# Optimization experiments

Measured on AMD Instinct MI355X. Metric: run time of the kernel, lower is better.

The kernel has to match this reference:

```python
import jax, jax.numpy as jnp
import numpy as np

N, E, F, H, L, G = 100000, 1600000, 32, 128, 4, 64


def gru_cell(m, h, w_ih, b_ih, w_hh, b_hh):
    # torch.nn.GRUCell math; gate order: r, z, n
    gi = m @ w_ih.T + b_ih          # [N, 3H]
    gh = h @ w_hh.T + b_hh          # [N, 3H]
    i_r, i_z, i_n = jnp.split(gi, 3, axis=-1)
    h_r, h_z, h_n = jnp.split(gh, 3, axis=-1)
    r = jax.nn.sigmoid(i_r + h_r)
    z = jax.nn.sigmoid(i_z + h_z)
    n = jnp.tanh(i_n + r * h_n)
    return (1.0 - z) * n + z * h


def setup_inputs() -> dict:
    key = jax.random.key(0)
    ks = jax.random.split(key, 12)
    s = 0.05
    return {
        "x": jax.random.normal(ks[0], (N, F), jnp.float32),
        "edge_index": jax.random.randint(ks[1], (2, E), 0, N, jnp.int64),
        "batch": jnp.sort(jax.random.randint(ks[2], (N,), 0, G, jnp.int64)),
        "num_graphs": G,
        "W0": jax.random.normal(ks[3], (H, F), jnp.float32) * s,
        "conv_w": jax.random.normal(ks[4], (L, H, H), jnp.float32) * s,
        "w_ih": jax.random.normal(ks[5], (3 * H, H), jnp.float32) * s,
        "b_ih": jax.random.normal(ks[6], (3 * H,), jnp.float32) * s,
        "w_hh": jax.random.normal(ks[7], (3 * H, H), jnp.float32) * s,
        "b_hh": jax.random.normal(ks[8], (3 * H,), jnp.float32) * s,
        "lin1_w": jax.random.normal(ks[9], (1, H), jnp.float32) * s,
        "lin1_b": jax.random.normal(ks[10], (1,), jnp.float32) * s,
    }


def reference(x, edge_index, batch, num_graphs, W0, conv_w, w_ih, b_ih, w_hh, b_hh, lin1_w, lin1_b):
    n_nodes = x.shape[0]
    # lin0 (no bias) + sigmoid embedding
    x_embed = jax.nn.sigmoid(x @ W0.T)                     # [N, H]

    src, dst = edge_index[0], edge_index[1]
    h = x_embed
    # GatedGraphConv: per layer, transform -> scatter-add over edges -> GRU update
    for l in range(conv_w.shape[0]):
        m = h @ conv_w[l]                                   # [N, H]
        agg = jax.ops.segment_sum(m[src], dst, num_segments=n_nodes)  # [N, H]
        h = gru_cell(agg, h, w_ih, b_ih, w_hh, b_hh)

    h = jax.nn.relu(h)
    out = h @ lin1_w.T + lin1_b                             # [N, 1]
    uncorrected = out

    # per-graph mean subtraction (scatter_mean + gather), same math as the loop
    sums = jax.ops.segment_sum(out, batch, num_segments=num_graphs)   # [G, 1]
    counts = jax.ops.segment_sum(jnp.ones((n_nodes, 1), out.dtype), batch, num_segments=num_graphs)
    mean_all = sums / jnp.maximum(counts, 1.0)
    corrected = out - mean_all[batch]

    return corrected.squeeze(1), x_embed, uncorrected.squeeze(1)
```

## Files before the change

### kernel.cpp

```cpp
#include <hip/hip_runtime.h>
#include <hip/hip_bf16.h>

#define HDIM 128
#define FDIM 32
#define GGR  64
#define SCAN_CHUNK 2048
#define FILL_CHUNK 1024
#define FILL_WIN 16

typedef __attribute__((ext_vector_type(8))) short bf16x8;
typedef __attribute__((ext_vector_type(4))) float f32x4;

__device__ __forceinline__ float fsig(float x) {
  return __builtin_amdgcn_rcpf(1.f + __expf(-x));
}
__device__ __forceinline__ float ftanh(float x) {
  return 1.f - 2.f * __builtin_amdgcn_rcpf(1.f + __expf(2.f * x));
}

__device__ __forceinline__ bf16x8 pack_bf16x8(float4 a, float4 b) {
  union { bf16x8 v; __hip_bfloat162 h[4]; } u;
  u.h[0] = __float22bfloat162_rn(make_float2(a.x, a.y));
  u.h[1] = __float22bfloat162_rn(make_float2(a.z, a.w));
  u.h[2] = __float22bfloat162_rn(make_float2(b.x, b.y));
  u.h[3] = __float22bfloat162_rn(make_float2(b.z, b.w));
  return u.v;
}

__device__ __forceinline__ int ablk(int kb, int m) {
  return (kb << 6) + (m & 56) + ((m ^ kb) & 7);
}

__device__ __forceinline__ void stage64(const unsigned short* __restrict__ g,
                                        short* __restrict__ s, int n0, int N, int t) {
#pragma unroll
  for (int r = 0; r < 2; ++r) {
    int idx = r * 512 + t;
    int m = idx >> 4, c8 = idx & 15;
    int gn = n0 + m;
    uint4 v = make_uint4(0u, 0u, 0u, 0u);
    if (gn < N) v = *(const uint4*)(g + (size_t)gn * HDIM + c8 * 8);
    *(uint4*)(s + ablk(c8, m) * 8) = v;
  }
}

__global__ __launch_bounds__(256) void k_embed_mfma(const float* __restrict__ x,
                                                    const unsigned short* __restrict__ W0b,
                                                    unsigned short* __restrict__ hb,
                                                    float* __restrict__ xemb,
                                                    const unsigned short* __restrict__ convT0,
                                                    unsigned short* __restrict__ m_out,
                                                    int N) {
  __shared__ short sE[16 * 64 * 8];
  int t = threadIdx.x;
  int w = t >> 6, l = t & 63;
  int lm = l & 15, lq = l >> 4;
  int n0 = blockIdx.x * 64;
  int j0 = w * 32;
  bf16x8 b0 = *(const bf16x8*)(W0b + (size_t)(j0 + lm) * FDIM + lq * 8);
  bf16x8 b1 = *(const bf16x8*)(W0b + (size_t)(j0 + 16 + lm) * FDIM + lq * 8);
  f32x4 acc0[4], acc1[4];
#pragma unroll
  for (int i = 0; i < 4; ++i) { acc0[i] = (f32x4){0.f,0.f,0.f,0.f}; acc1[i] = (f32x4){0.f,0.f,0.f,0.f}; }
#pragma unroll
  for (int tt = 0; tt < 4; ++tt) {
    int rg = n0 + tt * 16 + lm;
    bf16x8 a = (bf16x8){0,0,0,0,0,0,0,0};
    if (rg < N) {
      const float4* xr = (const float4*)x + (size_t)rg * 8 + lq * 2;
      a = pack_bf16x8(xr[0], xr[1]);
    }
    acc0[tt] = __builtin_amdgcn_mfma_f32_16x16x32_bf16(a, b0, acc0[tt], 0, 0, 0);
    acc1[tt] = __builtin_amdgcn_mfma_f32_16x16x32_bf16(a, b1, acc1[tt], 0, 0, 0);
  }
#pragma unroll
  for (int g = 0; g < 2; ++g) {
    int j = j0 + g * 16 + lm;
#pragma unroll
    for (int tt = 0; tt < 4; ++tt)
#pragma unroll
      for (int r = 0; r < 4; ++r) {
        int m = tt * 16 + lq * 4 + r;
        int node = n0 + m;
        float v = g ? acc1[tt][r] : acc0[tt][r];
        float e = fsig(v);
        __hip_bfloat16 eb = __float2bfloat16(e);
        ((__hip_bfloat16*)sE)[ablk(j >> 3, m) * 8 + (j & 7)] = eb;
        if (node < N) {
          size_t off = (size_t)node * HDIM + j;
          xemb[off] = e;
          ((__hip_bfloat16*)hb)[off] = eb;
        }
      }
  }
  __syncthreads();
#pragma unroll
  for (int g = 0; g < 2; ++g) {
    int jg = j0 + g * 16;
    f32x4 macc[4];
#pragma unroll
    for (int i = 0; i < 4; ++i) macc[i] = (f32x4){0.f,0.f,0.f,0.f};
#pragma unroll
    for (int ks = 0; ks < 4; ++ks) {
      bf16x8 b = *(const bf16x8*)(convT0 + (size_t)(jg + lm) * HDIM + ks * 32 + lq * 8);
      int kb = ks * 4 + lq;
#pragma unroll
      for (int tt = 0; tt < 4; ++tt) {
        bf16x8 a = *(const bf16x8*)(sE + ablk(kb, tt * 16 + lm) * 8);
        macc[tt] = __builtin_amdgcn_mfma_f32_16x16x32_bf16(a, b, macc[tt], 0, 0, 0);
      }
    }
    int j = jg + lm;
#pragma unroll
    for (int tt = 0; tt < 4; ++tt)
#pragma unroll
      for (int r = 0; r < 4; ++r) {
        int node = n0 + tt * 16 + lq * 4 + r;
        if (node < N)
          ((__hip_bfloat16*)m_out)[(size_t)node * HDIM + j] = __float2bfloat16(macc[tt][r]);
      }
  }
}

__global__ __launch_bounds__(256) void k_prep_w(const float* __restrict__ w_ih,
                                                const float* __restrict__ w_hh,
                                                const float* __restrict__ conv_w,
                                                const float* __restrict__ W0,
                                                unsigned short* __restrict__ wIb,
                                                unsigned short* __restrict__ wHb,
                                                unsigned short* __restrict__ convTb,
                                                unsigned short* __restrict__ W0b,
                                                int L) {
  int i = blockIdx.x * 256 + threadIdx.x;
  if (i < HDIM * FDIM) ((__hip_bfloat16*)W0b)[i] = __float2bfloat16(W0[i]);
  if (i < 384 * HDIM) {
    ((__hip_bfloat16*)wIb)[i] = __float2bfloat16(w_ih[i]);
    ((__hip_bfloat16*)wHb)[i] = __float2bfloat16(w_hh[i]);
  }
  int total = L * HDIM * HDIM;
  if (i < total) {
    int l = i >> 14, rem = i & 16383, j = rem >> 7, k = rem & 127;
    ((__hip_bfloat16*)convTb)[i] = __float2bfloat16(conv_w[(l << 14) + (k << 7) + j]);
  }
}

__global__ __launch_bounds__(256) void k_hist(const int* __restrict__ dst, int* __restrict__ deg,
                                              unsigned short* __restrict__ rank,
                                              long long E) {
  long long e = (long long)blockIdx.x * 256 + threadIdx.x;
  if (e < E) {
    int old = atomicAdd(&deg[dst[e]], 1);
    rank[e] = (unsigned short)old;
  }
}

__global__ __launch_bounds__(256) void k_block_sum(const int* __restrict__ deg,
                                                   int* __restrict__ bsum, int N) {
  int base = blockIdx.x * SCAN_CHUNK + threadIdx.x * 8;
  int s = 0;
#pragma unroll
  for (int u = 0; u < 8; ++u) { int i = base + u; if (i < N) s += deg[i]; }
#pragma unroll
  for (int o = 32; o; o >>= 1) s += __shfl_down(s, o, 64);
  __shared__ int wsum[4];
  if ((threadIdx.x & 63) == 0) wsum[threadIdx.x >> 6] = s;
  __syncthreads();
  if (threadIdx.x == 0) bsum[blockIdx.x] = wsum[0] + wsum[1] + wsum[2] + wsum[3];
}

__global__ void k_scan_bsums(int* __restrict__ bsum, int nb) {
  if (blockIdx.x == 0 && threadIdx.x == 0) {
    int run = 0;
    for (int i = 0; i < nb; ++i) { int v = bsum[i]; bsum[i] = run; run += v; }
  }
}

__global__ __launch_bounds__(256) void k_scan_chunks(const int* __restrict__ deg,
                                                     const int* __restrict__ bsum,
                                                     int* __restrict__ rowstart,
                                                     int N, int Etot) {
  __shared__ int ts[256];
  int base = blockIdx.x * SCAN_CHUNK + threadIdx.x * 8;
  int loc[8]; int s = 0;
#pragma unroll
  for (int u = 0; u < 8; ++u) {
    int i = base + u; loc[u] = s;
    s += (i < N) ? deg[i] : 0;
  }
  ts[threadIdx.x] = s;
  __syncthreads();
  for (int o = 1; o < 256; o <<= 1) {
    int v = (threadIdx.x >= o) ? ts[threadIdx.x - o] : 0;
    __syncthreads();
    ts[threadIdx.x] += v;
    __syncthreads();
  }
  int texcl = (threadIdx.x ? ts[threadIdx.x - 1] : 0) + bsum[blockIdx.x];
#pragma unroll
  for (int u = 0; u < 8; ++u) {
    int i = base + u;
    if (i < N) rowstart[i] = texcl + loc[u];
  }
  if (blockIdx.x == 0 && threadIdx.x == 0) rowstart[N] = Etot;
}

__global__ __launch_bounds__(256) void k_csr_fill_win(const int* __restrict__ src,
                                                      const int* __restrict__ dst,
                                                      const unsigned short* __restrict__ rank,
                                                      const int* __restrict__ rowstart,
                                                      int* __restrict__ csr,
                                                      long long E, int N) {
  __shared__ int sd[FILL_CHUNK];
  __shared__ int ss[FILL_CHUNK];
  __shared__ unsigned short sr[FILL_CHUNK];
  long long base = (long long)blockIdx.x * FILL_CHUNK;
  int cnt = (int)((E - base < FILL_CHUNK) ? (E - base) : FILL_CHUNK);
  for (int i = threadIdx.x; i < cnt; i += 256) {
    sd[i] = dst[base + i];
    ss[i] = src[base + i];
    sr[i] = rank[base + i];
  }
  __syncthreads();
  int nw = (N + FILL_WIN - 1) / FILL_WIN;
#pragma unroll 1
  for (int w = 0; w < FILL_WIN; ++w) {
    int lo = w * nw, hi = lo + nw;
    for (int i = threadIdx.x; i < cnt; i += 256) {
      int d = sd[i];
      if (d >= lo && d < hi)
        csr[rowstart[d] + sr[i]] = ss[i];
    }
    __syncthreads();
  }
}

__global__ __launch_bounds__(256) void k_gather(const int* __restrict__ csr,
                                                const int* __restrict__ rowstart,
                                                const unsigned short* __restrict__ m,
                                                unsigned short* __restrict__ agg, int N) {
  int wv = threadIdx.x >> 6, l = threadIdx.x & 63;
  int n = blockIdx.x * 4 + wv;
  if (n >= N) return;
  int eq = l >> 4;
  int jb = l & 15;
  int beg = rowstart[n], end = rowstart[n + 1];
  float acc[8] = {0.f, 0.f, 0.f, 0.f, 0.f, 0.f, 0.f, 0.f};
  for (int e0 = beg; e0 < end; e0 += 4) {
    int e = e0 + eq;
    uint4 v = make_uint4(0u, 0u, 0u, 0u);
    if (e < end) {
      int s = csr[e];
      v = *(const uint4*)(m + (size_t)s * HDIM + jb * 8);
    }
    acc[0] += __uint_as_float(v.x << 16);
    acc[1] += __uint_as_float(v.x & 0xffff0000u);
    acc[2] += __uint_as_float(v.y << 16);
    acc[3] += __uint_as_float(v.y & 0xffff0000u);
    acc[4] += __uint_as_float(v.z << 16);
    acc[5] += __uint_as_float(v.z & 0xffff0000u);
    acc[6] += __uint_as_float(v.w << 16);
    acc[7] += __uint_as_float(v.w & 0xffff0000u);
  }
#pragma unroll
  for (int i = 0; i < 8; ++i) {
    acc[i] += __shfl_xor(acc[i], 16, 64);
    acc[i] += __shfl_xor(acc[i], 32, 64);
  }
  if (eq == 0) {
    union { uint4 v; __hip_bfloat162 h[4]; } o;
#pragma unroll
    for (int i = 0; i < 4; ++i)
      o.h[i] = __float22bfloat162_rn(make_float2(acc[2 * i], acc[2 * i + 1]));
    *(uint4*)(agg + (size_t)n * HDIM + jb * 8) = o.v;
  }
}

__global__ __launch_bounds__(512) void k_gru_mfma(const unsigned short* __restrict__ aggb,
                                                  const unsigned short* __restrict__ hb,
                                                  const unsigned short* __restrict__ wI,
                                                  const unsigned short* __restrict__ wH,
                                                  const float* __restrict__ b_ih,
                                                  const float* __restrict__ b_hh,
                                                  unsigned short* __restrict__ hnewb,
                                                  const unsigned short* __restrict__ wT,
                                                  unsigned short* __restrict__ m_out,
                                                  int N) {
  __shared__ short sAg[16 * 64 * 8];
  __shared__ short sH[16 * 64 * 8];
  int t = threadIdx.x;
  int n0 = blockIdx.x * 64;
  stage64(aggb, sAg, n0, N, t);
  stage64(hb, sH, n0, N, t);
  int w = t >> 6, l = t & 63;
  int j0 = w * 16;
  int lm = l & 15, lq = l >> 4;
  int j = j0 + lm;
  float bir = b_ih[j], biz = b_ih[j + 128], bin = b_ih[j + 256];
  float bhr = b_hh[j], bhz = b_hh[j + 128], bhn = b_hh[j + 256];
  __syncthreads();
  f32x4 aIR[4], aIZ[4], aIN[4], aHR[4], aHZ[4], aHN[4];
#pragma unroll
  for (int i = 0; i < 4; ++i) {
    aIR[i] = (f32x4){0.f,0.f,0.f,0.f}; aIZ[i] = (f32x4){0.f,0.f,0.f,0.f};
    aIN[i] = (f32x4){0.f,0.f,0.f,0.f}; aHR[i] = (f32x4){0.f,0.f,0.f,0.f};
    aHZ[i] = (f32x4){0.f,0.f,0.f,0.f}; aHN[i] = (f32x4){0.f,0.f,0.f,0.f};
  }
#pragma unroll
  for (int ks = 0; ks < 4; ++ks) {
    size_t rI = (size_t)(j0 + lm) * HDIM + ks * 32 + lq * 8;
    bf16x8 bIr = *(const bf16x8*)(wI + rI);
    bf16x8 bIz = *(const bf16x8*)(wI + rI + 128 * HDIM);
    bf16x8 bIn = *(const bf16x8*)(wI + rI + 256 * HDIM);
    bf16x8 bHr = *(const bf16x8*)(wH + rI);
    bf16x8 bHz = *(const bf16x8*)(wH + rI + 128 * HDIM);
    bf16x8 bHn = *(const bf16x8*)(wH + rI + 256 * HDIM);
    int kb = ks * 4 + lq;
#pragma unroll
    for (int tt = 0; tt < 4; ++tt) {
      bf16x8 a = *(const bf16x8*)(sAg + ablk(kb, tt * 16 + lm) * 8);
      bf16x8 h = *(const bf16x8*)(sH + ablk(kb, tt * 16 + lm) * 8);
      aIR[tt] = __builtin_amdgcn_mfma_f32_16x16x32_bf16(a, bIr, aIR[tt], 0, 0, 0);
      aIZ[tt] = __builtin_amdgcn_mfma_f32_16x16x32_bf16(a, bIz, aIZ[tt], 0, 0, 0);
      aIN[tt] = __builtin_amdgcn_mfma_f32_16x16x32_bf16(a, bIn, aIN[tt], 0, 0, 0);
      aHR[tt] = __builtin_amdgcn_mfma_f32_16x16x32_bf16(h, bHr, aHR[tt], 0, 0, 0);
      aHZ[tt] = __builtin_amdgcn_mfma_f32_16x16x32_bf16(h, bHz, aHZ[tt], 0, 0, 0);
      aHN[tt] = __builtin_amdgcn_mfma_f32_16x16x32_bf16(h, bHn, aHN[tt], 0, 0, 0);
    }
  }
  __syncthreads();
#pragma unroll
  for (int tt = 0; tt < 4; ++tt)
#pragma unroll
    for (int r = 0; r < 4; ++r) {
      int m = tt * 16 + lq * 4 + r;
      int node = n0 + m;
      float hp = __bfloat162float(((const __hip_bfloat16*)sH)[ablk(j >> 3, m) * 8 + (j & 7)]);
      float rg = fsig(aIR[tt][r] + bir + aHR[tt][r] + bhr);
      float zg = fsig(aIZ[tt][r] + biz + aHZ[tt][r] + bhz);
      float nv = aIN[tt][r] + bin + rg * (aHN[tt][r] + bhn);
      float th = ftanh(nv);
      float hn = (1.f - zg) * th + zg * hp;
      __hip_bfloat16 hnb = __float2bfloat16(hn);
      ((__hip_bfloat16*)sAg)[ablk(j >> 3, m) * 8 + (j & 7)] = hnb;
      if (node < N)
        ((__hip_bfloat16*)hnewb)[(size_t)node * HDIM + j] = hnb;
    }
  if (wT) {
    __syncthreads();
    f32x4 macc[4];
#pragma unroll
    for (int i = 0; i < 4; ++i) macc[i] = (f32x4){0.f,0.f,0.f,0.f};
#pragma unroll
    for (int ks = 0; ks < 4; ++ks) {
      bf16x8 b = *(const bf16x8*)(wT + (size_t)(j0 + lm) * HDIM + ks * 32 + lq * 8);
      int kb = ks * 4 + lq;
#pragma unroll
      for (int tt = 0; tt < 4; ++tt) {
        bf16x8 a = *(const bf16x8*)(sAg + ablk(kb, tt * 16 + lm) * 8);
        macc[tt] = __builtin_amdgcn_mfma_f32_16x16x32_bf16(a, b, macc[tt], 0, 0, 0);
      }
    }
#pragma unroll
    for (int tt = 0; tt < 4; ++tt)
#pragma unroll
      for (int r = 0; r < 4; ++r) {
        int node = n0 + tt * 16 + lq * 4 + r;
        if (node < N)
          ((__hip_bfloat16*)m_out)[(size_t)node * HDIM + j] = __float2bfloat16(macc[tt][r]);
      }
  }
}

__global__ __launch_bounds__(256) void k_readout(const unsigned short* __restrict__ h,
                                                 const float* __restrict__ w1,
                                                 const float* __restrict__ b1,
                                                 float* __restrict__ out_raw,
                                                 float* __restrict__ uncorrected,
                                                 int N) {
  int wave = threadIdx.x >> 6;
  int lane = threadIdx.x & 63;
  int n = blockIdx.x * 4 + wave;
  if (n >= N) return;
  float h0 = __bfloat162float(((const __hip_bfloat16*)h)[(size_t)n * HDIM + lane]);
  float h1 = __bfloat162float(((const __hip_bfloat16*)h)[(size_t)n * HDIM + 64 + lane]);
  float v = fmaxf(h0, 0.f) * w1[lane] + fmaxf(h1, 0.f) * w1[64 + lane];
#pragma unroll
  for (int o = 32; o > 0; o >>= 1) v += __shfl_down(v, o, 64);
  if (lane == 0) {
    float o = v + b1[0];
    out_raw[n] = o;
    uncorrected[n] = o;
  }
}

__global__ __launch_bounds__(256) void k_graph_reduce(const float* __restrict__ out_raw,
                                                      const int* __restrict__ batch,
                                                      float* __restrict__ gsum,
                                                      float* __restrict__ gcnt,
                                                      int N) {
  __shared__ float ls[GGR], lc[GGR];
  int t = threadIdx.x;
  if (t < GGR) { ls[t] = 0.f; lc[t] = 0.f; }
  __syncthreads();
  for (int n = blockIdx.x * 256 + t; n < N; n += gridDim.x * 256) {
    int g = batch[n];
    atomicAdd(&ls[g], out_raw[n]);
    atomicAdd(&lc[g], 1.f);
  }
  __syncthreads();
  if (t < GGR) {
    unsafeAtomicAdd(&gsum[t], ls[t]);
    unsafeAtomicAdd(&gcnt[t], lc[t]);
  }
}

__global__ __launch_bounds__(256) void k_correct(const float* __restrict__ out_raw,
                                                 const int* __restrict__ batch,
                                                 const float* __restrict__ gsum,
                                                 const float* __restrict__ gcnt,
                                                 float* __restrict__ corrected, int N) {
  int n = blockIdx.x * 256 + threadIdx.x;
  if (n < N) {
    int g = batch[n];
    corrected[n] = out_raw[n] - gsum[g] / fmaxf(gcnt[g], 1.f);
  }
}

extern "C" void kernel_launch(void* const* d_in, const int* in_sizes, int n_in,
                              void* d_out, int out_size, void* d_ws, size_t ws_size,
                              hipStream_t stream) {
  const float* x      = (const float*)d_in[0];
  const int*   ei     = (const int*)d_in[1];
  const int*   batch  = (const int*)d_in[2];
  const float* W0     = (const float*)d_in[4];
  const float* conv_w = (const float*)d_in[5];
  const float* w_ih   = (const float*)d_in[6];
  const float* b_ih   = (const float*)d_in[7];
  const float* w_hh   = (const float*)d_in[8];
  const float* b_hh   = (const float*)d_in[9];
  const float* lin1_w = (const float*)d_in[10];
  const float* lin1_b = (const float*)d_in[11];

  int N = in_sizes[0] / FDIM;
  long long E = in_sizes[1] / 2;
  int L = in_sizes[5] / (HDIM * HDIM);

  const int* src = ei;
  const int* dstv = ei + E;

  float* out_corrected = (float*)d_out;
  float* out_xemb = out_corrected + N;
  float* out_unc  = out_xemb + (size_t)N * HDIM;

  char* p = (char*)d_ws;
  unsigned short* x0 = (unsigned short*)p; p += (size_t)N * HDIM * 2;
  unsigned short* x1 = (unsigned short*)p; p += (size_t)N * HDIM * 2;
  unsigned short* x2 = (unsigned short*)p; p += (size_t)N * HDIM * 2;
  float* out_raw = (float*)p;        p += (size_t)((N + 3) & ~3) * 4;
  float* gsum = (float*)p;           p += GGR * 4;
  float* gcnt = (float*)p;           p += GGR * 4;
  int* deg = (int*)p;                p += (size_t)((N + 3) & ~3) * 4;
  int* rowstart = (int*)p;           p += (size_t)(N + 4) * 4;
  int nb = (N + SCAN_CHUNK - 1) / SCAN_CHUNK;
  int* bsum = (int*)p;               p += (size_t)((nb + 63) & ~63) * 4;
  int* csr = (int*)p;                p += (size_t)E * 4;
  unsigned short* rankb = (unsigned short*)p;  p += (size_t)((E + 3) & ~3) * 2;
  unsigned short* wIb = (unsigned short*)p;    p += 384 * HDIM * 2;
  unsigned short* wHb = (unsigned short*)p;    p += 384 * HDIM * 2;
  unsigned short* convTb = (unsigned short*)p; p += (size_t)L * HDIM * HDIM * 2;
  unsigned short* W0b = (unsigned short*)p;

  int prep_total = (384 * HDIM > L * HDIM * HDIM) ? 384 * HDIM : L * HDIM * HDIM;
  k_prep_w<<<(prep_total + 255) / 256, 256, 0, stream>>>(w_ih, w_hh, conv_w, W0, wIb, wHb, convTb, W0b, L);

  hipMemsetAsync(deg, 0, (size_t)N * sizeof(int), stream);
  k_hist<<<(int)((E + 255) / 256), 256, 0, stream>>>(dstv, deg, rankb, E);
  k_block_sum<<<nb, 256, 0, stream>>>(deg, bsum, N);
  k_scan_bsums<<<1, 64, 0, stream>>>(bsum, nb);
  k_scan_chunks<<<nb, 256, 0, stream>>>(deg, bsum, rowstart, N, (int)E);
  k_csr_fill_win<<<(int)((E + FILL_CHUNK - 1) / FILL_CHUNK), 256, 0, stream>>>(
      src, dstv, rankb, rowstart, csr, E, N);

  int nblk = (N + 63) / 64;
  k_embed_mfma<<<nblk, 256, 0, stream>>>(x, W0b, x0, out_xemb, convTb, x1, N);

  unsigned short* Hb = x0;
  unsigned short* Mb = x1;
  for (int l = 0; l < L; ++l) {
    k_gather<<<(N + 3) / 4, 256, 0, stream>>>(csr, rowstart, Mb, x2, N);
    const unsigned short* wTn = (l + 1 < L) ? (convTb + (size_t)(l + 1) * HDIM * HDIM) : nullptr;
    k_gru_mfma<<<nblk, 512, 0, stream>>>(x2, Hb, wIb, wHb, b_ih, b_hh, Mb, wTn, Hb, N);
    unsigned short* tmp = Hb; Hb = Mb; Mb = tmp;
  }

  hipMemsetAsync(gsum, 0, 2 * GGR * sizeof(float), stream);
  k_readout<<<(N + 3) / 4, 256, 0, stream>>>(Hb, lin1_w, lin1_b, out_raw, out_unc, N);
  k_graph_reduce<<<256, 256, 0, stream>>>(out_raw, batch, gsum, gcnt, N);
  k_correct<<<(N + 255) / 256, 256, 0, stream>>>(out_raw, batch, gsum, gcnt, out_corrected, N);
}
```

Measured before the change: 844.9 us.

## Fuse histogram into embed kernel; merge GRU accumulators and raise occupancy

```diff
diff --git a/kernel.cpp b/kernel.cpp
--- a/kernel.cpp
+++ b/kernel.cpp
@@ -44,18 +44,31 @@
   }
 }
 
-__global__ __launch_bounds__(256) void k_embed_mfma(const float* __restrict__ x,
+__global__ __launch_bounds__(256) void k_embed_hist(const float* __restrict__ x,
                                                     const unsigned short* __restrict__ W0b,
                                                     unsigned short* __restrict__ hb,
                                                     float* __restrict__ xemb,
                                                     const unsigned short* __restrict__ convT0,
                                                     unsigned short* __restrict__ m_out,
-                                                    int N) {
+                                                    int N,
+                                                    const int* __restrict__ dst,
+                                                    int* __restrict__ deg,
+                                                    unsigned short* __restrict__ rank,
+                                                    long long E, int histBlocks) {
   __shared__ short sE[16 * 64 * 8];
+  if ((int)blockIdx.x < histBlocks) {
+    long long e = (long long)blockIdx.x * 256 + threadIdx.x;
+    if (e < E) {
+      int old = atomicAdd(&deg[dst[e]], 1);
+      rank[e] = (unsigned short)old;
+    }
+    return;
+  }
+  int bid = blockIdx.x - histBlocks;
   int t = threadIdx.x;
   int w = t >> 6, l = t & 63;
   int lm = l & 15, lq = l >> 4;
-  int n0 = blockIdx.x * 64;
+  int n0 = bid * 64;
   int j0 = w * 32;
   bf16x8 b0 = *(const bf16x8*)(W0b + (size_t)(j0 + lm) * FDIM + lq * 8);
   bf16x8 b1 = *(const bf16x8*)(W0b + (size_t)(j0 + 16 + lm) * FDIM + lq * 8);
@@ -141,16 +154,6 @@
   if (i < total) {
     int l = i >> 14, rem = i & 16383, j = rem >> 7, k = rem & 127;
     ((__hip_bfloat16*)convTb)[i] = __float2bfloat16(conv_w[(l << 14) + (k << 7) + j]);
-  }
-}
-
-__global__ __launch_bounds__(256) void k_hist(const int* __restrict__ dst, int* __restrict__ deg,
-                                              unsigned short* __restrict__ rank,
-                                              long long E) {
-  long long e = (long long)blockIdx.x * 256 + threadIdx.x;
-  if (e < E) {
-    int old = atomicAdd(&deg[dst[e]], 1);
-    rank[e] = (unsigned short)old;
   }
 }
 
@@ -275,7 +278,7 @@
   }
 }
 
-__global__ __launch_bounds__(512) void k_gru_mfma(const unsigned short* __restrict__ aggb,
+__global__ __launch_bounds__(512, 4) void k_gru_mfma(const unsigned short* __restrict__ aggb,
                                                   const unsigned short* __restrict__ hb,
                                                   const unsigned short* __restrict__ wI,
                                                   const unsigned short* __restrict__ wH,
@@ -298,12 +301,11 @@
   float bir = b_ih[j], biz = b_ih[j + 128], bin = b_ih[j + 256];
   float bhr = b_hh[j], bhz = b_hh[j + 128], bhn = b_hh[j + 256];
   __syncthreads();
-  f32x4 aIR[4], aIZ[4], aIN[4], aHR[4], aHZ[4], aHN[4];
+  f32x4 aR[4], aZ[4], aNi[4], aNh[4];
 #pragma unroll
   for (int i = 0; i < 4; ++i) {
-    aIR[i] = (f32x4){0.f,0.f,0.f,0.f}; aIZ[i] = (f32x4){0.f,0.f,0.f,0.f};
-    aIN[i] = (f32x4){0.f,0.f,0.f,0.f}; aHR[i] = (f32x4){0.f,0.f,0.f,0.f};
-    aHZ[i] = (f32x4){0.f,0.f,0.f,0.f}; aHN[i] = (f32x4){0.f,0.f,0.f,0.f};
+    aR[i] = (f32x4){0.f,0.f,0.f,0.f}; aZ[i] = (f32x4){0.f,0.f,0.f,0.f};
+    aNi[i] = (f32x4){0.f,0.f,0.f,0.f}; aNh[i] = (f32x4){0.f,0.f,0.f,0.f};
   }
 #pragma unroll
   for (int ks = 0; ks < 4; ++ks) {
@@ -319,12 +321,12 @@
     for (int tt = 0; tt < 4; ++tt) {
       bf16x8 a = *(const bf16x8*)(sAg + ablk(kb, tt * 16 + lm) * 8);
       bf16x8 h = *(const bf16x8*)(sH + ablk(kb, tt * 16 + lm) * 8);
-      aIR[tt] = __builtin_amdgcn_mfma_f32_16x16x32_bf16(a, bIr, aIR[tt], 0, 0, 0);
-      aIZ[tt] = __builtin_amdgcn_mfma_f32_16x16x32_bf16(a, bIz, aIZ[tt], 0, 0, 0);
-      aIN[tt] = __builtin_amdgcn_mfma_f32_16x16x32_bf16(a, bIn, aIN[tt], 0, 0, 0);
-      aHR[tt] = __builtin_amdgcn_mfma_f32_16x16x32_bf16(h, bHr, aHR[tt], 0, 0, 0);
-      aHZ[tt] = __builtin_amdgcn_mfma_f32_16x16x32_bf16(h, bHz, aHZ[tt], 0, 0, 0);
-      aHN[tt] = __builtin_amdgcn_mfma_f32_16x16x32_bf16(h, bHn, aHN[tt], 0, 0, 0);
+      aR[tt] = __builtin_amdgcn_mfma_f32_16x16x32_bf16(a, bIr, aR[tt], 0, 0, 0);
+      aR[tt] = __builtin_amdgcn_mfma_f32_16x16x32_bf16(h, bHr, aR[tt], 0, 0, 0);
+      aZ[tt] = __builtin_amdgcn_mfma_f32_16x16x32_bf16(a, bIz, aZ[tt], 0, 0, 0);
+      aZ[tt] = __builtin_amdgcn_mfma_f32_16x16x32_bf16(h, bHz, aZ[tt], 0, 0, 0);
+      aNi[tt] = __builtin_amdgcn_mfma_f32_16x16x32_bf16(a, bIn, aNi[tt], 0, 0, 0);
+      aNh[tt] = __builtin_amdgcn_mfma_f32_16x16x32_bf16(h, bHn, aNh[tt], 0, 0, 0);
     }
   }
   __syncthreads();
@@ -335,9 +337,9 @@
       int m = tt * 16 + lq * 4 + r;
       int node = n0 + m;
       float hp = __bfloat162float(((const __hip_bfloat16*)sH)[ablk(j >> 3, m) * 8 + (j & 7)]);
-      float rg = fsig(aIR[tt][r] + bir + aHR[tt][r] + bhr);
-      float zg = fsig(aIZ[tt][r] + biz + aHZ[tt][r] + bhz);
-      float nv = aIN[tt][r] + bin + rg * (aHN[tt][r] + bhn);
+      float rg = fsig(aR[tt][r] + bir + bhr);
+      float zg = fsig(aZ[tt][r] + biz + bhz);
+      float nv = aNi[tt][r] + bin + rg * (aNh[tt][r] + bhn);
       float th = ftanh(nv);
       float hn = (1.f - zg) * th + zg * hp;
       __hip_bfloat16 hnb = __float2bfloat16(hn);
@@ -474,15 +476,17 @@
   k_prep_w<<<(prep_total + 255) / 256, 256, 0, stream>>>(w_ih, w_hh, conv_w, W0, wIb, wHb, convTb, W0b, L);
 
   hipMemsetAsync(deg, 0, (size_t)N * sizeof(int), stream);
-  k_hist<<<(int)((E + 255) / 256), 256, 0, stream>>>(dstv, deg, rankb, E);
+
+  int nblk = (N + 63) / 64;
+  int histBlocks = (int)((E + 255) / 256);
+  k_embed_hist<<<histBlocks + nblk, 256, 0, stream>>>(x, W0b, x0, out_xemb, convTb, x1, N,
+                                                      dstv, deg, rankb, E, histBlocks);
+
   k_block_sum<<<nb, 256, 0, stream>>>(deg, bsum, N);
   k_scan_bsums<<<1, 64, 0, stream>>>(bsum, nb);
   k_scan_chunks<<<nb, 256, 0, stream>>>(deg, bsum, rowstart, N, (int)E);
   k_csr_fill_win<<<(int)((E + FILL_CHUNK - 1) / FILL_CHUNK), 256, 0, stream>>>(
       src, dstv, rankb, rowstart, csr, E, N);
-
-  int nblk = (N + 63) / 64;
-  k_embed_mfma<<<nblk, 256, 0, stream>>>(x, W0b, x0, out_xemb, convTb, x1, N);
 
   unsigned short* Hb = x0;
   unsigned short* Mb = x1;
```

After: 774.0 us. 8.4% less time.
